# Performance work log

Measured on AMD Instinct MI355X. Metric: run time of the kernel, lower is better.

Reference implementation:

```python
import jax, jax.numpy as jnp
import numpy as np
import math

V, T, E, H, L = 32000, 1024, 1024, 16, 6
B = 2
D = E // H
F = 4 * E


def setup_inputs() -> dict:
    key = jax.random.key(0)
    ks = jax.random.split(key, 12)
    s = 0.02
    rn = lambda k, shape: jax.random.normal(k, shape, jnp.float32) * s
    return dict(
        idx=jax.random.randint(ks[0], (B, T), 0, V),
        tok_w=rn(ks[1], (V, E)),
        pos_w=rn(ks[2], (T, E)),
        ln1_g=jnp.ones((L, E)), ln1_b=jnp.zeros((L, E)),
        wq=rn(ks[3], (L, E, E)), wk=rn(ks[4], (L, E, E)), wv=rn(ks[5], (L, E, E)),
        wp=rn(ks[6], (L, E, E)), bp=jnp.zeros((L, E)),
        ln2_g=jnp.ones((L, E)), ln2_b=jnp.zeros((L, E)),
        w1=rn(ks[7], (L, E, F)), b1=jnp.zeros((L, F)),
        w2=rn(ks[8], (L, F, E)), b2=jnp.zeros((L, E)),
        lnf_g=jnp.ones((E,)), lnf_b=jnp.zeros((E,)),
        wlm=rn(ks[9], (E, V)), blm=jnp.zeros((V,)),
    )


def _layernorm(x, g, b, eps=1e-5):
    m = jnp.mean(x, axis=-1, keepdims=True)
    v = jnp.var(x, axis=-1, keepdims=True)
    return (x - m) * jax.lax.rsqrt(v + eps) * g + b


def _forward(idx, tok_w, pos_w, ln1_g, ln1_b, wq, wk, wv, wp, bp,
             ln2_g, ln2_b, w1, b1, w2, b2, lnf_g, lnf_b, wlm, blm):
    Bx, Tx = idx.shape
    x = tok_w[idx] + pos_w[jnp.arange(Tx)][None, :, :]  # [B,T,E]
    causal = jnp.tril(jnp.ones((Tx, Tx), dtype=bool))
    scale = 1.0 / math.sqrt(D)
    for l in range(L):
        h = _layernorm(x, ln1_g[l], ln1_b[l])
        q = (h @ wq[l]).reshape(Bx, Tx, H, D).transpose(0, 2, 1, 3)  # [B,H,T,D]
        k = (h @ wk[l]).reshape(Bx, Tx, H, D).transpose(0, 2, 1, 3)
        v = (h @ wv[l]).reshape(Bx, Tx, H, D).transpose(0, 2, 1, 3)
        att = jnp.einsum('bhtd,bhsd->bhts', q, k) * scale  # [B,H,T,T]
        att = jnp.where(causal, att, -jnp.inf)
        att = jax.nn.softmax(att, axis=-1)
        y = jnp.einsum('bhts,bhsd->bhtd', att, v)
        y = y.transpose(0, 2, 1, 3).reshape(Bx, Tx, E)
        x = x + y @ wp[l] + bp[l]
        h2 = _layernorm(x, ln2_g[l], ln2_b[l])
        ff = jax.nn.gelu(h2 @ w1[l] + b1[l], approximate=False) @ w2[l] + b2[l]
        x = x + ff
    x = _layernorm(x, lnf_g, lnf_b)
    return x @ wlm + blm  # logits [B,T,V]


def reference(idx, tok_w, pos_w, ln1_g, ln1_b, wq, wk, wv, wp, bp,
              ln2_g, ln2_b, w1, b1, w2, b2, lnf_g, lnf_b, wlm, blm):
    return _forward(idx, tok_w, pos_w, ln1_g, ln1_b, wq, wk, wv, wp, bp,
                    ln2_g, ln2_b, w1, b1, w2, b2, lnf_g, lnf_b, wlm, blm)
```

## Files before the change

### kernel.cpp

```cpp
#include <hip/hip_runtime.h>

#define T_SEQ   1024
#define E_DIM   1024
#define H_HEADS 16
#define D_HEAD  64
#define L_LAYERS 6
#define B_BATCH 2
#define F_DIM   4096
#define V_VOCAB 32000

typedef float f32x4 __attribute__((ext_vector_type(4)));
typedef short short8 __attribute__((ext_vector_type(8)));

__device__ __forceinline__ unsigned short f2bf(float f) {
  union { float f; unsigned int u; } v; v.f = f;
  unsigned int r = v.u + 0x7fffu + ((v.u >> 16) & 1u);
  return (unsigned short)(r >> 16);
}

#define GLDS16(gp, lp) __builtin_amdgcn_global_load_lds( \
    (const __attribute__((address_space(1))) void*)(gp), \
    (__attribute__((address_space(3))) void*)(lp), 16, 0, 0)

__global__ void embed_kernel(const int* __restrict__ idx, const float* __restrict__ tok,
                             const float* __restrict__ pos, float* __restrict__ x) {
  int i = blockIdx.x * 256 + threadIdx.x;
  int bt = i >> 8;
  int e4 = i & 255;
  int t  = bt & (T_SEQ - 1);
  int tokid = idx[bt];
  f32x4 a = *(const f32x4*)(tok + (size_t)tokid * E_DIM + e4 * 4);
  f32x4 p = *(const f32x4*)(pos + (size_t)t * E_DIM + e4 * 4);
  *(f32x4*)(x + (size_t)bt * E_DIM + e4 * 4) = a + p;
}

__global__ void ln_kernel(const float* __restrict__ x, const float* __restrict__ g,
                          const float* __restrict__ b, unsigned short* __restrict__ out) {
  int row = blockIdx.x;
  int tid = threadIdx.x;
  const float* xr = x + (size_t)row * E_DIM;
  f32x4 v = *(const f32x4*)(xr + tid * 4);
  float s  = v[0] + v[1] + v[2] + v[3];
  float s2 = v[0]*v[0] + v[1]*v[1] + v[2]*v[2] + v[3]*v[3];
  #pragma unroll
  for (int off = 32; off > 0; off >>= 1) {
    s  += __shfl_xor(s,  off);
    s2 += __shfl_xor(s2, off);
  }
  __shared__ float red[2][4];
  int wave = tid >> 6;
  if ((tid & 63) == 0) { red[0][wave] = s; red[1][wave] = s2; }
  __syncthreads();
  s  = red[0][0] + red[0][1] + red[0][2] + red[0][3];
  s2 = red[1][0] + red[1][1] + red[1][2] + red[1][3];
  float mean = s * (1.0f / E_DIM);
  float var  = s2 * (1.0f / E_DIM) - mean * mean;
  float rstd = rsqrtf(var + 1e-5f);
  f32x4 gv = *(const f32x4*)(g + tid * 4);
  f32x4 bv = *(const f32x4*)(b + tid * 4);
  ushort4 o;
  o.x = f2bf((v[0] - mean) * rstd * gv[0] + bv[0]);
  o.y = f2bf((v[1] - mean) * rstd * gv[1] + bv[1]);
  o.z = f2bf((v[2] - mean) * rstd * gv[2] + bv[2]);
  o.w = f2bf((v[3] - mean) * rstd * gv[3] + bv[3]);
  *(ushort4*)(out + (size_t)row * E_DIM + tid * 4) = o;
}

__device__ __forceinline__ void wtrans_body(const float* __restrict__ W,
    unsigned short* __restrict__ Wt, int K, int N, int bx, int by) {
  __shared__ float tile[64][65];
  const int n0 = bx * 64, k0 = by * 64;
  const int tr  = threadIdx.x >> 4;
  const int tc4 = (threadIdx.x & 15) * 4;
  #pragma unroll
  for (int p = 0; p < 4; ++p) {
    f32x4 v = *(const f32x4*)(W + (size_t)(k0 + p * 16 + tr) * N + n0 + tc4);
    tile[p * 16 + tr][tc4 + 0] = v[0];
    tile[p * 16 + tr][tc4 + 1] = v[1];
    tile[p * 16 + tr][tc4 + 2] = v[2];
    tile[p * 16 + tr][tc4 + 3] = v[3];
  }
  __syncthreads();
  #pragma unroll
  for (int p = 0; p < 4; ++p) {
    int n = p * 16 + tr;
    ushort4 o;
    o.x = f2bf(tile[tc4 + 0][n]);
    o.y = f2bf(tile[tc4 + 1][n]);
    o.z = f2bf(tile[tc4 + 2][n]);
    o.w = f2bf(tile[tc4 + 3][n]);
    *(ushort4*)(Wt + (size_t)(n0 + n) * K + k0 + tc4) = o;
  }
}

__global__ __launch_bounds__(256) void wtrans_kernel(const float* __restrict__ W,
    unsigned short* __restrict__ Wt, int K, int N) {
  wtrans_body(W, Wt, K, N, blockIdx.x, blockIdx.y);
}

__global__ __launch_bounds__(256) void wtrans6_kernel(const float* __restrict__ wq,
    const float* __restrict__ wk, const float* __restrict__ wv, const float* __restrict__ wp,
    const float* __restrict__ w1, const float* __restrict__ w2,
    unsigned short* __restrict__ wtb) {
  const size_t EE = (size_t)E_DIM * E_DIM;
  const size_t EF = (size_t)E_DIM * F_DIM;
  const int id = blockIdx.x;
  if (id < 1024) {
    const int z = id >> 8, r = id & 255;
    const float* W = z == 0 ? wq : (z == 1 ? wk : (z == 2 ? wv : wp));
    wtrans_body(W, wtb + z * EE, E_DIM, E_DIM, r & 15, r >> 4);
  } else if (id < 2048) {
    const int r = id - 1024;
    wtrans_body(w1, wtb + 4 * EE, E_DIM, F_DIM, r & 63, r >> 6);
  } else {
    const int r = id - 2048;
    wtrans_body(w2, wtb + 4 * EE + EF, F_DIM, E_DIM, r & 15, r >> 4);
  }
}

__global__ __launch_bounds__(512) void attn_mfma_kernel(
    const unsigned short* __restrict__ qk, const unsigned short* __restrict__ vt,
    unsigned short* __restrict__ y) {
  __shared__ __align__(16) char smem[2 * 16384 + 8 * 1280 + 512];
  const int tid  = threadIdx.x;
  const int lane = tid & 63;
  const int wave = tid >> 6;
  const int wl = wave & 3;
  const int g  = wave >> 2;
  const int qx = blockIdx.x;
  const int h  = blockIdx.y & (H_HEADS - 1);
  const int b  = blockIdx.y >> 4;
  const int qt = b ? (15 - qx) : qx;
  const int r0 = qt * 64 + wl * 16;
  const size_t RS = 2 * E_DIM;
  const unsigned short* q  = qk + (size_t)b * T_SEQ * RS + (size_t)h * D_HEAD;
  const unsigned short* k  = q + E_DIM;
  const unsigned short* vb = vt + (size_t)(b * H_HEADS + h) * D_HEAD * T_SEQ;
  const size_t ybase = (size_t)b * T_SEQ * E_DIM + (size_t)h * D_HEAD;
  const int fr = lane & 15, fg = lane >> 4;
  const int srow = lane >> 3;
  const int ssw  = ((lane & 7) * 16) ^ (srow << 4);
  char* pb = smem + 32768 + wave * 1280;
  float* mlb = (float*)(smem + 32768 + 10240);

  short8 aq[2];
  #pragma unroll
  for (int c = 0; c < 2; ++c)
    aq[c] = *(const short8*)(q + (size_t)(r0 + fr) * RS + c * 32 + fg * 8);

  f32x4 oacc[4];
  #pragma unroll
  for (int cg = 0; cg < 4; ++cg) oacc[cg] = (f32x4){0.f, 0.f, 0.f, 0.f};
  float m_ = -1e30f, l_ = 0.0f;

  auto stage = [&](int t) {
    const int j0 = t * 64;
    char* Kd = smem + (t & 1) * 16384;
    GLDS16((const char*)k  + (size_t)(j0 + wave * 8 + srow) * RS * 2 + ssw,
           Kd + wave * 1024);
    GLDS16((const char*)vb + ((size_t)(wave * 8 + srow) * T_SEQ + j0) * 2 + ssw,
           Kd + 8192 + wave * 1024);
  };

  stage(0);
  for (int t = 0; t <= qt; ++t) {
    __builtin_amdgcn_sched_barrier(0);
    __builtin_amdgcn_s_barrier();
    if (t < qt) stage(t + 1);
    __builtin_amdgcn_sched_barrier(0);
    if (t < qt) asm volatile("s_waitcnt vmcnt(2)" ::: "memory");
    else        asm volatile("s_waitcnt vmcnt(0)" ::: "memory");
    __builtin_amdgcn_sched_barrier(0);
    __builtin_amdgcn_s_barrier();
    __builtin_amdgcn_sched_barrier(0);
    const char* Kl = smem + (t & 1) * 16384;
    const char* Vl = Kl + 8192;
    const int j0 = t * 64;
    if (!(t == qt && g == 1 && wl < 2)) {
      f32x4 st[2];
      #pragma unroll
      for (int cc = 0; cc < 2; ++cc) {
        const int kloc = g * 32 + cc * 16 + fr;
        const char* kb = Kl + kloc * 128;
        const int sw = (kloc & 7) << 4;
        short8 ka0 = *(const short8*)(kb + ((fg * 16) ^ sw));
        short8 ka1 = *(const short8*)(kb + ((64 + fg * 16) ^ sw));
        f32x4 z = (f32x4){0.f, 0.f, 0.f, 0.f};
        z = __builtin_amdgcn_mfma_f32_16x16x32_bf16(ka0, aq[0], z, 0, 0, 0);
        z = __builtin_amdgcn_mfma_f32_16x16x32_bf16(ka1, aq[1], z, 0, 0, 0);
        st[cc] = z;
      }
      const int qg = r0 + fr;
      float pv[2][4];
      float mx = -1e30f;
      #pragma unroll
      for (int cc = 0; cc < 2; ++cc)
        #pragma unroll
        for (int r = 0; r < 4; ++r) {
          const int kj = j0 + g * 32 + cc * 16 + fg * 4 + r;
          float val = (kj <= qg) ? st[cc][r] * 0.125f : -1e30f;
          pv[cc][r] = val;
          mx = fmaxf(mx, val);
        }
      mx = fmaxf(mx, __shfl_xor(mx, 16));
      mx = fmaxf(mx, __shfl_xor(mx, 32));
      const float mn = fmaxf(m_, mx);
      const float cfs = __expf(m_ - mn);
      float ls = 0.0f;
      #pragma unroll
      for (int cc = 0; cc < 2; ++cc) {
        ushort4 o;
        float e0 = pv[cc][0] > -1e29f ? __expf(pv[cc][0] - mn) : 0.0f;
        float e1 = pv[cc][1] > -1e29f ? __expf(pv[cc][1] - mn) : 0.0f;
        float e2 = pv[cc][2] > -1e29f ? __expf(pv[cc][2] - mn) : 0.0f;
        float e3 = pv[cc][3] > -1e29f ? __expf(pv[cc][3] - mn) : 0.0f;
        ls += (e0 + e1) + (e2 + e3);
        o.x = f2bf(e0); o.y = f2bf(e1); o.z = f2bf(e2); o.w = f2bf(e3);
        *(ushort4*)(pb + fr * 80 + cc * 32 + fg * 8) = o;
      }
      ls += __shfl_xor(ls, 16);
      ls += __shfl_xor(ls, 32);
      l_ = l_ * cfs + ls;
      m_ = mn;
      float cfO[4];
      #pragma unroll
      for (int r = 0; r < 4; ++r) cfO[r] = __shfl(cfs, (lane & 48) | (fg * 4 + r));
      asm volatile("s_waitcnt lgkmcnt(0)" ::: "memory");
      __builtin_amdgcn_sched_barrier(0);
      short8 pa = *(const short8*)(pb + fr * 80 + fg * 16);
      __builtin_amdgcn_s_setprio(1);
      #pragma unroll
      for (int cg = 0; cg < 4; ++cg) {
        const int d = cg * 16 + fr;
        short8 bv = *(const short8*)(Vl + d * 128 + ((g * 64 + fg * 16) ^ ((d & 7) << 4)));
        #pragma unroll
        for (int r = 0; r < 4; ++r) oacc[cg][r] *= cfO[r];
        oacc[cg] = __builtin_amdgcn_mfma_f32_16x16x32_bf16(pa, bv, oacc[cg], 0, 0, 0);
      }
      __builtin_amdgcn_s_setprio(0);
    }
  }
  __syncthreads();
  float* obuf = (float*)smem;
  if (g == 1) {
    #pragma unroll
    for (int cg = 0; cg < 4; ++cg)
      #pragma unroll
      for (int r = 0; r < 4; ++r)
        obuf[wl * 1024 + (fg * 4 + r) * 64 + cg * 16 + fr] = oacc[cg][r];
    if (fg == 0) { mlb[(wl * 16 + fr) * 2] = m_; mlb[(wl * 16 + fr) * 2 + 1] = l_; }
  }
  __syncthreads();
  if (g == 0) {
    const float m1 = mlb[(wl * 16 + fr) * 2];
    const float l1 = mlb[(wl * 16 + fr) * 2 + 1];
    const float m  = fmaxf(m_, m1);
    const float c0 = __expf(m_ - m), c1 = __expf(m1 - m);
    const float li = 1.0f / (l_ * c0 + l1 * c1);
    float c0O[4], c1O[4], liO[4];
    #pragma unroll
    for (int r = 0; r < 4; ++r) {
      const int src = (lane & 48) | (fg * 4 + r);
      c0O[r] = __shfl(c0, src); c1O[r] = __shfl(c1, src); liO[r] = __shfl(li, src);
    }
    #pragma unroll
    for (int cg = 0; cg < 4; ++cg)
      #pragma unroll
      for (int r = 0; r < 4; ++r) {
        const float o1 = obuf[wl * 1024 + (fg * 4 + r) * 64 + cg * 16 + fr];
        const float val = (oacc[cg][r] * c0O[r] + o1 * c1O[r]) * liO[r];
        y[ybase + (size_t)(r0 + fg * 4 + r) * E_DIM + cg * 16 + fr] = f2bf(val);
      }
  }
}

template<int BM, int BN, bool HAS_BIAS, bool GELU_ACT, bool HAS_RES, int OMODE>
__global__ __launch_bounds__(256) void gemm_bt_kernel(
    const unsigned short* __restrict__ A, const unsigned short* __restrict__ Bt,
    const float* __restrict__ bias, const float* __restrict__ res,
    void* __restrict__ out, unsigned short* __restrict__ vt, int M, int N, int K) {
  constexpr int BK = 64;
  constexpr int MR = BM / 32;
  constexpr int NR = BN / 32;
  constexpr int AI = BM / 32;
  constexpr int BI = BN / 32;
  __shared__ __align__(16) unsigned short As[BM * BK];
  __shared__ __align__(16) unsigned short Bs[BN * BK];
  const int tid  = threadIdx.x;
  const int lane = tid & 63;
  const int wave = tid >> 6;
  const int wr = wave >> 1, wc = wave & 1;

  const int mt = M / BM;
  const int q8 = gridDim.x >> 3;
  const int g  = (blockIdx.x & 7) * q8 + (blockIdx.x >> 3);
  const int m0 = (g % mt) * BM, n0 = (g / mt) * BN;

  const int fr = lane & 15, fg = lane >> 4;
  const int lrow = lane >> 3;
  const int scol = ((lane & 7) * 16) ^ (lrow << 4);
  const size_t K2 = (size_t)K * 2;
  const char* aG = (const char*)A  + (size_t)(m0 + wave * 8 + lrow) * K2 + scol;
  const char* bG = (const char*)Bt + (size_t)(n0 + wave * 8 + lrow) * K2 + scol;

  f32x4 acc[MR][NR];
  #pragma unroll
  for (int mi = 0; mi < MR; ++mi)
    #pragma unroll
    for (int ni = 0; ni < NR; ++ni) acc[mi][ni] = (f32x4){0.f, 0.f, 0.f, 0.f};

  for (int k0 = 0; k0 < K; k0 += BK) {
    __syncthreads();
    #pragma unroll
    for (int i = 0; i < AI; ++i)
      GLDS16(aG + (size_t)i * 32 * K2 + (size_t)k0 * 2, (char*)As + wave * 1024 + i * 4096);
    #pragma unroll
    for (int i = 0; i < BI; ++i)
      GLDS16(bG + (size_t)i * 32 * K2 + (size_t)k0 * 2, (char*)Bs + wave * 1024 + i * 4096);
    __syncthreads();

    short8 af[MR][2], bf[NR][2];
    #pragma unroll
    for (int mi = 0; mi < MR; ++mi) {
      const int row = wr * (BM / 2) + mi * 16 + fr;
      #pragma unroll
      for (int kh = 0; kh < 2; ++kh)
        af[mi][kh] = *(const short8*)((const char*)As + row * 128 +
                       ((kh * 64 + fg * 16) ^ ((row & 7) << 4)));
    }
    #pragma unroll
    for (int ni = 0; ni < NR; ++ni) {
      const int row = wc * (BN / 2) + ni * 16 + fr;
      #pragma unroll
      for (int kh = 0; kh < 2; ++kh)
        bf[ni][kh] = *(const short8*)((const char*)Bs + row * 128 +
                       ((kh * 64 + fg * 16) ^ ((row & 7) << 4)));
    }
    #pragma unroll
    for (int mi = 0; mi < MR; ++mi)
      #pragma unroll
      for (int ni = 0; ni < NR; ++ni) {
        acc[mi][ni] = __builtin_amdgcn_mfma_f32_16x16x32_bf16(af[mi][0], bf[ni][0], acc[mi][ni], 0, 0, 0);
        acc[mi][ni] = __builtin_amdgcn_mfma_f32_16x16x32_bf16(af[mi][1], bf[ni][1], acc[mi][ni], 0, 0, 0);
      }
  }

  #pragma unroll
  for (int mi = 0; mi < MR; ++mi) {
    #pragma unroll
    for (int ni = 0; ni < NR; ++ni) {
      const int col = n0 + wc * (BN / 2) + ni * 16 + fr;
      float bv = HAS_BIAS ? bias[col] : 0.0f;
      float vals[4];
      const int rbase = m0 + wr * (BM / 2) + mi * 16 + fg * 4;
      #pragma unroll
      for (int r = 0; r < 4; ++r) {
        float val = acc[mi][ni][r] + bv;
        if (GELU_ACT) val = 0.5f * val * (1.0f + erff(val * 0.70710678118f));
        if (HAS_RES)  val += res[(size_t)(rbase + r) * N + col];
        vals[r] = val;
      }
      if (OMODE == 0) {
        #pragma unroll
        for (int r = 0; r < 4; ++r)
          ((float*)out)[(size_t)(rbase + r) * N + col] = vals[r];
      } else {
        #pragma unroll
        for (int r = 0; r < 4; ++r)
          ((unsigned short*)out)[(size_t)(rbase + r) * N + col] = f2bf(vals[r]);
      }
    }
  }
}

template<int OMODE, bool HAS_BIAS, bool GELU_ACT>
__global__ __launch_bounds__(512, 1) void gemm8p2_kernel(
    const unsigned short* __restrict__ A, const unsigned short* __restrict__ Bt,
    const float* __restrict__ bias, void* __restrict__ out,
    unsigned short* __restrict__ vt, int M, int N, int K) {
  __shared__ __align__(16) char lds[98304];
  const int tid  = threadIdx.x;
  const int lane = tid & 63;
  const int wv   = tid >> 6;
  const int wm = wv >> 2, wn = wv & 3;

  const int mt = M >> 7;
  const int q8 = gridDim.x >> 3;
  const int g  = (blockIdx.x & 7) * q8 + (blockIdx.x >> 3);
  const int m0 = (g % mt) * 128, n0 = (g / mt) * 256;

  const int fr = lane & 15, fg = lane >> 4;
  const size_t K2 = (size_t)K * 2;
  const int nIter = K >> 7;

  const int csw0 = (fg * 16) ^ ((fr & 7) << 4);
  const int csw1 = (64 + fg * 16) ^ ((fr & 7) << 4);

  const int sc = (lane * 16) & 127;
  const size_t laneoff = (size_t)(lane >> 3) * K2 + (size_t)(sc ^ ((lane >> 3) << 4));
  const char* Asrc = (const char*)(A + (size_t)m0 * K) + laneoff;
  const char* Bsrc = (const char*)(Bt + (size_t)n0 * K) + laneoff;
  const int arow_wv = (wv >> 2) * 64 + (wv & 3) * 8;
  const int brow_wv = (wv >> 2) * 64 + (wv & 3) * 8;

  f32x4 acc[4][4];
  #pragma unroll
  for (int i = 0; i < 4; ++i)
    #pragma unroll
    for (int j = 0; j < 4; ++j) acc[i][j] = (f32x4){0.f, 0.f, 0.f, 0.f};

  auto stageA = [&](int b, int c, int kt) {
    GLDS16(Asrc + (size_t)(arow_wv + c * 32) * K2 + (size_t)kt * 128,
           lds + b * 49152 + c * 8192 + wv * 1024);
  };
  auto stageB = [&](int b, int j, int kt) {
    GLDS16(Bsrc + (size_t)((j & 1) * 128 + (j >> 1) * 32 + brow_wv) * K2 + (size_t)kt * 128,
           lds + b * 49152 + 16384 + j * 8192 + wv * 1024);
  };

  stageA(0, 0, 0); stageA(0, 1, 0);
  stageB(0, 0, 0); stageB(0, 1, 0); stageB(0, 2, 0); stageB(0, 3, 0);
  stageA(1, 0, 1); stageB(1, 0, 1); stageB(1, 1, 1);
  __builtin_amdgcn_sched_barrier(0);
  asm volatile("s_waitcnt vmcnt(3)" ::: "memory");
  __builtin_amdgcn_s_barrier();

  for (int i = 0; i < nIter; ++i) {
    const bool last = (i == nIter - 1);
    #pragma unroll
    for (int p = 0; p < 8; ++p) {
      const int b  = p >> 2;
      const int mh = (p >> 1) & 1;
      const int nh = p & 1;
      const char* Ab = lds + b * 49152;
      const char* Bb = Ab + 16384;
      __builtin_amdgcn_sched_barrier(0);
      short8 fa[2][2], fb[2][2];
      #pragma unroll
      for (int j = 0; j < 2; ++j) {
        const int row = mh * 64 + wm * 32 + j * 16 + fr;
        fa[j][0] = *(const short8*)(Ab + row * 128 + csw0);
        fa[j][1] = *(const short8*)(Ab + row * 128 + csw1);
      }
      #pragma unroll
      for (int n = 0; n < 2; ++n) {
        const int row = nh * 128 + (wn >> 1) * 64 + (wn & 1) * 32 + n * 16 + fr;
        fb[n][0] = *(const short8*)(Bb + row * 128 + csw0);
        fb[n][1] = *(const short8*)(Bb + row * 128 + csw1);
      }
      if (p == 0) stageA(1, 1, 2 * i + 1);
      if (p == 1) { stageB(1, 2, 2 * i + 1); stageB(1, 3, 2 * i + 1); }
      if (!last) {
        if (p == 2) stageA(0, 0, 2 * i + 2);
        if (p == 3) { stageB(0, 0, 2 * i + 2); stageB(0, 1, 2 * i + 2); }
        if (p == 4) stageA(0, 1, 2 * i + 2);
        if (p == 5) { stageB(0, 2, 2 * i + 2); stageB(0, 3, 2 * i + 2); }
        if (p == 6) stageA(1, 0, 2 * i + 3);
        if (p == 7) { stageB(1, 0, 2 * i + 3); stageB(1, 1, 2 * i + 3); }
      }
      __builtin_amdgcn_sched_barrier(0);
      __builtin_amdgcn_s_barrier();
      __builtin_amdgcn_sched_barrier(0);
      __builtin_amdgcn_s_setprio(1);
      #pragma unroll
      for (int j = 0; j < 2; ++j)
        #pragma unroll
        for (int n = 0; n < 2; ++n) {
          acc[mh * 2 + j][nh * 2 + n] = __builtin_amdgcn_mfma_f32_16x16x32_bf16(
              fa[j][0], fb[n][0], acc[mh * 2 + j][nh * 2 + n], 0, 0, 0);
          acc[mh * 2 + j][nh * 2 + n] = __builtin_amdgcn_mfma_f32_16x16x32_bf16(
              fa[j][1], fb[n][1], acc[mh * 2 + j][nh * 2 + n], 0, 0, 0);
        }
      __builtin_amdgcn_s_setprio(0);
      __builtin_amdgcn_sched_barrier(0);
      if (p == 3) {
        if (!last) asm volatile("s_waitcnt vmcnt(3)" ::: "memory");
        else       asm volatile("s_waitcnt vmcnt(0)" ::: "memory");
      }
      if (p == 7 && !last)
        asm volatile("s_waitcnt vmcnt(3)" ::: "memory");
      __builtin_amdgcn_s_barrier();
    }
  }

  #pragma unroll
  for (int mi = 0; mi < 4; ++mi) {
    #pragma unroll
    for (int ni = 0; ni < 4; ++ni) {
      const int col = n0 + wn * 64 + ni * 16 + fr;
      float bv = HAS_BIAS ? bias[col] : 0.0f;
      const int rbase = m0 + wm * 64 + mi * 16 + fg * 4;
      float vals[4];
      #pragma unroll
      for (int r = 0; r < 4; ++r) {
        float val = acc[mi][ni][r] + bv;
        if (GELU_ACT) val = 0.5f * val * (1.0f + erff(val * 0.70710678118f));
        vals[r] = val;
      }
      if (OMODE == 1) {
        #pragma unroll
        for (int r = 0; r < 4; ++r)
          ((unsigned short*)out)[(size_t)(rbase + r) * N + col] = f2bf(vals[r]);
      } else {
        if (col < 2 * E_DIM) {
          #pragma unroll
          for (int r = 0; r < 4; ++r)
            ((unsigned short*)out)[(size_t)(rbase + r) * 2 * E_DIM + col] = f2bf(vals[r]);
        } else {
          const int c2 = col - 2 * E_DIM;
          const int hh = c2 >> 6, d = c2 & 63;
          const int bb = rbase >> 10, t0 = rbase & (T_SEQ - 1);
          ushort4 o;
          o.x = f2bf(vals[0]); o.y = f2bf(vals[1]);
          o.z = f2bf(vals[2]); o.w = f2bf(vals[3]);
          *(ushort4*)(vt + ((size_t)(bb * H_HEADS + hh) * D_HEAD + d) * T_SEQ + t0) = o;
        }
      }
    }
  }
}

__global__ __launch_bounds__(512, 1) void gemm8p_kernel(
    const unsigned short* __restrict__ A, const unsigned short* __restrict__ Bt,
    const float* __restrict__ bias, float* __restrict__ out, int M, int N, int K) {
  __shared__ __align__(16) char lds[131072];
  const int tid  = threadIdx.x;
  const int lane = tid & 63;
  const int wv   = tid >> 6;
  const int wm = wv >> 2, wn = wv & 3;

  const int mt = M >> 8;
  const int q8 = gridDim.x >> 3;
  const int g  = (blockIdx.x & 7) * q8 + (blockIdx.x >> 3);
  const int m0 = (g % mt) * 256, n0 = (g / mt) * 256;

  const int fr = lane & 15, fg = lane >> 4;
  const size_t K2 = (size_t)K * 2;
  const int nIter = K >> 7;

  const int csw0 = (fg * 16) ^ ((fr & 7) << 4);
  const int csw1 = (64 + fg * 16) ^ ((fr & 7) << 4);

  const int sc = (lane * 16) & 127;
  const size_t laneoff = (size_t)(lane >> 3) * K2 + (size_t)(sc ^ ((lane >> 3) << 4));
  const char* Asrc = (const char*)(A + (size_t)m0 * K) + (size_t)(wv * 8) * K2 + laneoff;
  const char* Bsrc = (const char*)(Bt + (size_t)n0 * K) + laneoff;

  f32x4 acc[8][4];
  #pragma unroll
  for (int i = 0; i < 8; ++i)
    #pragma unroll
    for (int j = 0; j < 4; ++j) acc[i][j] = (f32x4){0.f, 0.f, 0.f, 0.f};

  auto stageA = [&](int b, int q, int kt) {
    GLDS16(Asrc + (size_t)(q * 64) * K2 + (size_t)kt * 128,
           lds + b * 65536 + q * 8192 + wv * 1024);
  };
  auto stageB = [&](int b, int j, int o, int kt) {
    const int gw = j * 64 + wv * 8;
    const int rw = ((gw >> 5) << 6) + (gw & 31) + o * 32;
    GLDS16(Bsrc + (size_t)rw * K2 + (size_t)kt * 128,
           lds + b * 65536 + 32768 + rw * 128);
  };

  stageA(0, 0, 0); stageA(0, 2, 0);
  stageB(0, 0, 0, 0); stageB(0, 1, 0, 0);
  stageA(0, 1, 0); stageA(0, 3, 0);
  stageB(0, 0, 1, 0); stageB(0, 1, 1, 0);
  stageA(1, 0, 1); stageA(1, 2, 1);
  stageB(1, 0, 0, 1); stageB(1, 1, 0, 1);
  __builtin_amdgcn_sched_barrier(0);
  asm volatile("s_waitcnt vmcnt(4)" ::: "memory");
  __builtin_amdgcn_s_barrier();

  for (int i = 0; i < nIter; ++i) {
    const bool last = (i == nIter - 1);
    #pragma unroll
    for (int p = 0; p < 8; ++p) {
      const int b  = p >> 2;
      const int mh = (p & 3) >> 1;
      const int nh = p & 1;
      const char* Ab = lds + b * 65536;
      const char* Bb = Ab + 32768;
      __builtin_amdgcn_sched_barrier(0);
      short8 fa[4][2], fb[2][2];
      #pragma unroll
      for (int j = 0; j < 4; ++j) {
        const int row = wm * 128 + mh * 64 + j * 16 + fr;
        fa[j][0] = *(const short8*)(Ab + row * 128 + csw0);
        fa[j][1] = *(const short8*)(Ab + row * 128 + csw1);
      }
      #pragma unroll
      for (int n = 0; n < 2; ++n) {
        const int row = wn * 64 + nh * 32 + n * 16 + fr;
        fb[n][0] = *(const short8*)(Bb + row * 128 + csw0);
        fb[n][1] = *(const short8*)(Bb + row * 128 + csw1);
      }
      if (p == 0) { stageA(1, 1, 2 * i + 1); stageA(1, 3, 2 * i + 1); }
      if (p == 1) { stageB(1, 0, 1, 2 * i + 1); stageB(1, 1, 1, 2 * i + 1); }
      if (!last) {
        if (p == 2) { stageA(0, 0, 2 * i + 2); stageA(0, 2, 2 * i + 2); }
        if (p == 3) { stageB(0, 0, 0, 2 * i + 2); stageB(0, 1, 0, 2 * i + 2); }
        if (p == 4) { stageA(0, 1, 2 * i + 2); stageA(0, 3, 2 * i + 2); }
        if (p == 5) { stageB(0, 0, 1, 2 * i + 2); stageB(0, 1, 1, 2 * i + 2); }
        if (p == 6) { stageA(1, 0, 2 * i + 3); stageA(1, 2, 2 * i + 3); }
        if (p == 7) { stageB(1, 0, 0, 2 * i + 3); stageB(1, 1, 0, 2 * i + 3); }
      }
      __builtin_amdgcn_sched_barrier(0);
      __builtin_amdgcn_s_barrier();
      __builtin_amdgcn_sched_barrier(0);
      __builtin_amdgcn_s_setprio(1);
      #pragma unroll
      for (int j = 0; j < 4; ++j)
        #pragma unroll
        for (int n = 0; n < 2; ++n) {
          acc[mh * 4 + j][nh * 2 + n] = __builtin_amdgcn_mfma_f32_16x16x32_bf16(
              fa[j][0], fb[n][0], acc[mh * 4 + j][nh * 2 + n], 0, 0, 0);
          acc[mh * 4 + j][nh * 2 + n] = __builtin_amdgcn_mfma_f32_16x16x32_bf16(
              fa[j][1], fb[n][1], acc[mh * 4 + j][nh * 2 + n], 0, 0, 0);
        }
      __builtin_amdgcn_s_setprio(0);
      __builtin_amdgcn_sched_barrier(0);
      if (p == 3) {
        if (!last) asm volatile("s_waitcnt vmcnt(4)" ::: "memory");
        else       asm volatile("s_waitcnt vmcnt(0)" ::: "memory");
      }
      if (p == 7 && !last)
        asm volatile("s_waitcnt vmcnt(4)" ::: "memory");
      __builtin_amdgcn_s_barrier();
    }
  }

  #pragma unroll
  for (int mi = 0; mi < 8; ++mi) {
    #pragma unroll
    for (int ni = 0; ni < 4; ++ni) {
      const int col = n0 + wn * 64 + ni * 16 + fr;
      const float bv = bias[col];
      #pragma unroll
      for (int r = 0; r < 4; ++r) {
        const int row = m0 + wm * 128 + mi * 16 + fg * 4 + r;
        out[(size_t)row * N + col] = acc[mi][ni][r] + bv;
      }
    }
  }
}

extern "C" void kernel_launch(void* const* d_in, const int* in_sizes, int n_in,
                              void* d_out, int out_size, void* d_ws, size_t ws_size,
                              hipStream_t stream) {
  const int*   idx   = (const int*)  d_in[0];
  const float* tok_w = (const float*)d_in[1];
  const float* pos_w = (const float*)d_in[2];
  const float* ln1_g = (const float*)d_in[3];
  const float* ln1_b = (const float*)d_in[4];
  const float* wq    = (const float*)d_in[5];
  const float* wk    = (const float*)d_in[6];
  const float* wv    = (const float*)d_in[7];
  const float* wp    = (const float*)d_in[8];
  const float* bp    = (const float*)d_in[9];
  const float* ln2_g = (const float*)d_in[10];
  const float* ln2_b = (const float*)d_in[11];
  const float* w1    = (const float*)d_in[12];
  const float* b1    = (const float*)d_in[13];
  const float* w2    = (const float*)d_in[14];
  const float* b2    = (const float*)d_in[15];
  const float* lnf_g = (const float*)d_in[16];
  const float* lnf_b = (const float*)d_in[17];
  const float* wlm   = (const float*)d_in[18];
  const float* blm   = (const float*)d_in[19];

  const int M = B_BATCH * T_SEQ;
  const size_t EE = (size_t)E_DIM * E_DIM;
  const size_t EF = (size_t)E_DIM * F_DIM;
  char* p = (char*)d_ws;
  float* x            = (float*)p;          p += (size_t)M * E_DIM * 4;
  unsigned short* hb  = (unsigned short*)p; p += (size_t)M * E_DIM * 2;
  unsigned short* qkb = (unsigned short*)p; p += (size_t)M * 2 * E_DIM * 2;
  unsigned short* vtb = (unsigned short*)p; p += (size_t)M * E_DIM * 2;
  unsigned short* yb  = (unsigned short*)p; p += (size_t)M * E_DIM * 2;
  unsigned short* tb  = (unsigned short*)p; p += (size_t)M * F_DIM * 2;
  unsigned short* wtb = (unsigned short*)p; p += (size_t)V_VOCAB * E_DIM * 2;

  embed_kernel<<<M * E_DIM / 4 / 256, 256, 0, stream>>>(idx, tok_w, pos_w, x);

  for (int l = 0; l < L_LAYERS; ++l) {
    wtrans6_kernel<<<3072, 256, 0, stream>>>(
        wq + l * EE, wk + l * EE, wv + l * EE, wp + l * EE,
        w1 + l * EF, w2 + l * EF, wtb);
    ln_kernel<<<M, 256, 0, stream>>>(x, ln1_g + (size_t)l * E_DIM, ln1_b + (size_t)l * E_DIM, hb);
    gemm8p2_kernel<2, false, false>
        <<<(M / 128) * (3 * E_DIM / 256), 512, 0, stream>>>(
        hb, wtb, nullptr, qkb, vtb, M, 3 * E_DIM, E_DIM);
    attn_mfma_kernel<<<dim3(16, B_BATCH * H_HEADS), 512, 0, stream>>>(qkb, vtb, yb);
    gemm_bt_kernel<64, 128, true, false, true, 0>
        <<<(M / 64) * (E_DIM / 128), 256, 0, stream>>>(
        yb, wtb + 3 * EE, bp + (size_t)l * E_DIM, x, x, nullptr, M, E_DIM, E_DIM);
    ln_kernel<<<M, 256, 0, stream>>>(x, ln2_g + (size_t)l * E_DIM, ln2_b + (size_t)l * E_DIM, hb);
    gemm8p2_kernel<1, true, true>
        <<<(M / 128) * (F_DIM / 256), 512, 0, stream>>>(
        hb, wtb + 4 * EE, b1 + (size_t)l * F_DIM, tb, nullptr, M, F_DIM, E_DIM);
    gemm_bt_kernel<64, 128, true, false, true, 0>
        <<<(M / 64) * (E_DIM / 128), 256, 0, stream>>>(
        tb, wtb + 4 * EE + EF, b2 + (size_t)l * E_DIM, x, x, nullptr, M, E_DIM, F_DIM);
  }
  ln_kernel<<<M, 256, 0, stream>>>(x, lnf_g, lnf_b, hb);
  wtrans_kernel<<<dim3(V_VOCAB / 64, E_DIM / 64), 256, 0, stream>>>(wlm, wtb, E_DIM, V_VOCAB);
  gemm8p_kernel<<<(M / 256) * (V_VOCAB / 256), 512, 0, stream>>>(
      hb, wtb, blm, (float*)d_out, M, V_VOCAB, E_DIM);
}
```

Before: 1.297 ms.

## Stage GEMM epilogues through LDS for vector stores; merge layernorm into weight-transpose launches

Rewrites the epilogues of the three GEMM kernels so each wave first writes its accumulator tile into a padded LDS scratch area. It then reads the tile back row-wise and emits 16-byte (fp32) or 8-byte (bf16) vectorised global stores, with vectorised residual loads, instead of scattered scalar stores. Separately, the layernorm launches are folded into the weight-transpose kernels as extra blocks, both per layer and for the final LM head, removing kernel launches. This adds LDS reuse after the main loop, with explicit waitcnt and sched barriers, and makes the grids heterogeneous.

New measurement: 1.292 ms. Within noise of the previous version (-0.4%).

```diff
diff --git a/kernel.cpp b/kernel.cpp
--- a/kernel.cpp
+++ b/kernel.cpp
@@ -34,9 +34,9 @@
   *(f32x4*)(x + (size_t)bt * E_DIM + e4 * 4) = a + p;
 }
 
-__global__ void ln_kernel(const float* __restrict__ x, const float* __restrict__ g,
-                          const float* __restrict__ b, unsigned short* __restrict__ out) {
-  int row = blockIdx.x;
+__device__ __forceinline__ void ln_body(const float* __restrict__ x,
+    const float* __restrict__ g, const float* __restrict__ b,
+    unsigned short* __restrict__ out, int row) {
   int tid = threadIdx.x;
   const float* xr = x + (size_t)row * E_DIM;
   f32x4 v = *(const f32x4*)(xr + tid * 4);
@@ -66,6 +66,11 @@
   *(ushort4*)(out + (size_t)row * E_DIM + tid * 4) = o;
 }
 
+__global__ void ln_kernel(const float* __restrict__ x, const float* __restrict__ g,
+                          const float* __restrict__ b, unsigned short* __restrict__ out) {
+  ln_body(x, g, b, out, blockIdx.x);
+}
+
 __device__ __forceinline__ void wtrans_body(const float* __restrict__ W,
     unsigned short* __restrict__ Wt, int K, int N, int bx, int by) {
   __shared__ float tile[64][65];
@@ -93,15 +98,12 @@
   }
 }
 
-__global__ __launch_bounds__(256) void wtrans_kernel(const float* __restrict__ W,
-    unsigned short* __restrict__ Wt, int K, int N) {
-  wtrans_body(W, Wt, K, N, blockIdx.x, blockIdx.y);
-}
-
-__global__ __launch_bounds__(256) void wtrans6_kernel(const float* __restrict__ wq,
+__global__ __launch_bounds__(256) void wtrans6ln_kernel(const float* __restrict__ wq,
     const float* __restrict__ wk, const float* __restrict__ wv, const float* __restrict__ wp,
     const float* __restrict__ w1, const float* __restrict__ w2,
-    unsigned short* __restrict__ wtb) {
+    const float* __restrict__ lng, const float* __restrict__ lnb,
+    const float* __restrict__ x, unsigned short* __restrict__ wtb,
+    unsigned short* __restrict__ hb) {
   const size_t EE = (size_t)E_DIM * E_DIM;
   const size_t EF = (size_t)E_DIM * F_DIM;
   const int id = blockIdx.x;
@@ -112,10 +114,21 @@
   } else if (id < 2048) {
     const int r = id - 1024;
     wtrans_body(w1, wtb + 4 * EE, E_DIM, F_DIM, r & 63, r >> 6);
-  } else {
+  } else if (id < 3072) {
     const int r = id - 2048;
     wtrans_body(w2, wtb + 4 * EE + EF, F_DIM, E_DIM, r & 15, r >> 4);
-  }
+  } else {
+    ln_body(x, lng, lnb, hb, id - 3072);
+  }
+}
+
+__global__ __launch_bounds__(256) void wtransv_ln_kernel(const float* __restrict__ wlm,
+    const float* __restrict__ lng, const float* __restrict__ lnb,
+    const float* __restrict__ x, unsigned short* __restrict__ wtb,
+    unsigned short* __restrict__ hb) {
+  const int id = blockIdx.x;
+  if (id < 8000) wtrans_body(wlm, wtb, E_DIM, V_VOCAB, id % 500, id / 500);
+  else           ln_body(x, lng, lnb, hb, id - 8000);
 }
 
 __global__ __launch_bounds__(512) void attn_mfma_kernel(
@@ -284,8 +297,9 @@
   constexpr int NR = BN / 32;
   constexpr int AI = BM / 32;
   constexpr int BI = BN / 32;
-  __shared__ __align__(16) unsigned short As[BM * BK];
-  __shared__ __align__(16) unsigned short Bs[BN * BK];
+  __shared__ __align__(16) char smem[(BM + BN) * BK * 2];
+  unsigned short* As = (unsigned short*)smem;
+  unsigned short* Bs = (unsigned short*)(smem + (size_t)BM * BK * 2);
   const int tid  = threadIdx.x;
   const int lane = tid & 63;
   const int wave = tid >> 6;
@@ -345,31 +359,52 @@
       }
   }
 
-  #pragma unroll
-  for (int mi = 0; mi < MR; ++mi) {
-    #pragma unroll
-    for (int ni = 0; ni < NR; ++ni) {
-      const int col = n0 + wc * (BN / 2) + ni * 16 + fr;
-      float bv = HAS_BIAS ? bias[col] : 0.0f;
-      float vals[4];
-      const int rbase = m0 + wr * (BM / 2) + mi * 16 + fg * 4;
-      #pragma unroll
-      for (int r = 0; r < 4; ++r) {
-        float val = acc[mi][ni][r] + bv;
-        if (GELU_ACT) val = 0.5f * val * (1.0f + erff(val * 0.70710678118f));
-        if (HAS_RES)  val += res[(size_t)(rbase + r) * N + col];
-        vals[r] = val;
-      }
-      if (OMODE == 0) {
+  if (OMODE == 0) {
+    __syncthreads();
+    float* tw = (float*)(smem + wave * 4352);
+    float bv4[NR];
+    #pragma unroll
+    for (int ni = 0; ni < NR; ++ni)
+      bv4[ni] = HAS_BIAS ? bias[n0 + wc * (BN / 2) + ni * 16 + fr] : 0.0f;
+    #pragma unroll
+    for (int mi = 0; mi < MR; ++mi) {
+      #pragma unroll
+      for (int ni = 0; ni < NR; ++ni)
         #pragma unroll
-        for (int r = 0; r < 4; ++r)
-          ((float*)out)[(size_t)(rbase + r) * N + col] = vals[r];
-      } else {
+        for (int r = 0; r < 4; ++r) {
+          float val = acc[mi][ni][r] + bv4[ni];
+          if (GELU_ACT) val = 0.5f * val * (1.0f + erff(val * 0.70710678118f));
+          tw[(fg * 4 + r) * 68 + ni * 16 + fr] = val;
+        }
+      asm volatile("s_waitcnt lgkmcnt(0)" ::: "memory");
+      __builtin_amdgcn_sched_barrier(0);
+      #pragma unroll
+      for (int rr = 0; rr < 4; ++rr) {
+        const int row = rr * 4 + (lane >> 4);
+        const int grow = m0 + wr * (BM / 2) + mi * 16 + row;
+        const int gcol = n0 + wc * (BN / 2) + (lane & 15) * 4;
+        f32x4 v = *(const f32x4*)&tw[row * 68 + (lane & 15) * 4];
+        if (HAS_RES) v += *(const f32x4*)(res + (size_t)grow * N + gcol);
+        *(f32x4*)((float*)out + (size_t)grow * N + gcol) = v;
+      }
+      asm volatile("s_waitcnt lgkmcnt(0)" ::: "memory");
+      __builtin_amdgcn_sched_barrier(0);
+    }
+  } else {
+    #pragma unroll
+    for (int mi = 0; mi < MR; ++mi)
+      #pragma unroll
+      for (int ni = 0; ni < NR; ++ni) {
+        const int col = n0 + wc * (BN / 2) + ni * 16 + fr;
+        float bv = HAS_BIAS ? bias[col] : 0.0f;
+        const int rbase = m0 + wr * (BM / 2) + mi * 16 + fg * 4;
         #pragma unroll
-        for (int r = 0; r < 4; ++r)
-          ((unsigned short*)out)[(size_t)(rbase + r) * N + col] = f2bf(vals[r]);
-      }
-    }
+        for (int r = 0; r < 4; ++r) {
+          float val = acc[mi][ni][r] + bv;
+          if (GELU_ACT) val = 0.5f * val * (1.0f + erff(val * 0.70710678118f));
+          ((unsigned short*)out)[(size_t)(rbase + r) * N + col] = f2bf(val);
+        }
+      }
   }
 }
 
@@ -483,25 +518,46 @@
     }
   }
 
-  #pragma unroll
-  for (int mi = 0; mi < 4; ++mi) {
-    #pragma unroll
-    for (int ni = 0; ni < 4; ++ni) {
-      const int col = n0 + wn * 64 + ni * 16 + fr;
-      float bv = HAS_BIAS ? bias[col] : 0.0f;
-      const int rbase = m0 + wm * 64 + mi * 16 + fg * 4;
-      float vals[4];
-      #pragma unroll
-      for (int r = 0; r < 4; ++r) {
-        float val = acc[mi][ni][r] + bv;
-        if (GELU_ACT) val = 0.5f * val * (1.0f + erff(val * 0.70710678118f));
-        vals[r] = val;
-      }
-      if (OMODE == 1) {
+  if (OMODE == 1) {
+    unsigned short* tw = (unsigned short*)(lds + wv * 2176);
+    float bv4[4];
+    #pragma unroll
+    for (int ni = 0; ni < 4; ++ni)
+      bv4[ni] = HAS_BIAS ? bias[n0 + wn * 64 + ni * 16 + fr] : 0.0f;
+    #pragma unroll
+    for (int mi = 0; mi < 4; ++mi) {
+      #pragma unroll
+      for (int ni = 0; ni < 4; ++ni)
         #pragma unroll
-        for (int r = 0; r < 4; ++r)
-          ((unsigned short*)out)[(size_t)(rbase + r) * N + col] = f2bf(vals[r]);
-      } else {
+        for (int r = 0; r < 4; ++r) {
+          float val = acc[mi][ni][r] + bv4[ni];
+          if (GELU_ACT) val = 0.5f * val * (1.0f + erff(val * 0.70710678118f));
+          tw[(fg * 4 + r) * 68 + ni * 16 + fr] = f2bf(val);
+        }
+      asm volatile("s_waitcnt lgkmcnt(0)" ::: "memory");
+      __builtin_amdgcn_sched_barrier(0);
+      #pragma unroll
+      for (int rr = 0; rr < 4; ++rr) {
+        const int row = rr * 4 + (lane >> 4);
+        const int grow = m0 + wm * 64 + mi * 16 + row;
+        const int gcol = n0 + wn * 64 + (lane & 15) * 4;
+        ushort4 v = *(const ushort4*)&tw[row * 68 + (lane & 15) * 4];
+        *(ushort4*)((unsigned short*)out + (size_t)grow * N + gcol) = v;
+      }
+      asm volatile("s_waitcnt lgkmcnt(0)" ::: "memory");
+      __builtin_amdgcn_sched_barrier(0);
+    }
+  } else {
+    #pragma unroll
+    for (int mi = 0; mi < 4; ++mi) {
+      #pragma unroll
+      for (int ni = 0; ni < 4; ++ni) {
+        const int col = n0 + wn * 64 + ni * 16 + fr;
+        float bv = HAS_BIAS ? bias[col] : 0.0f;
+        const int rbase = m0 + wm * 64 + mi * 16 + fg * 4;
+        float vals[4];
+        #pragma unroll
+        for (int r = 0; r < 4; ++r) vals[r] = acc[mi][ni][r] + bv;
         if (col < 2 * E_DIM) {
           #pragma unroll
           for (int r = 0; r < 4; ++r)
@@ -631,18 +687,29 @@
     }
   }
 
+  float* tw = (float*)(lds + wv * 4352);
+  float bv4[4];
+  #pragma unroll
+  for (int ni = 0; ni < 4; ++ni) bv4[ni] = bias[n0 + wn * 64 + ni * 16 + fr];
   #pragma unroll
   for (int mi = 0; mi < 8; ++mi) {
     #pragma unroll
-    for (int ni = 0; ni < 4; ++ni) {
-      const int col = n0 + wn * 64 + ni * 16 + fr;
-      const float bv = bias[col];
-      #pragma unroll
-      for (int r = 0; r < 4; ++r) {
-        const int row = m0 + wm * 128 + mi * 16 + fg * 4 + r;
-        out[(size_t)row * N + col] = acc[mi][ni][r] + bv;
-      }
-    }
+    for (int ni = 0; ni < 4; ++ni)
+      #pragma unroll
+      for (int r = 0; r < 4; ++r)
+        tw[(fg * 4 + r) * 68 + ni * 16 + fr] = acc[mi][ni][r] + bv4[ni];
+    asm volatile("s_waitcnt lgkmcnt(0)" ::: "memory");
+    __builtin_amdgcn_sched_barrier(0);
+    #pragma unroll
+    for (int rr = 0; rr < 4; ++rr) {
+      const int row = rr * 4 + (lane >> 4);
+      const int grow = m0 + wm * 128 + mi * 16 + row;
+      const int gcol = n0 + wn * 64 + (lane & 15) * 4;
+      f32x4 v = *(const f32x4*)&tw[row * 68 + (lane & 15) * 4];
+      *(f32x4*)(out + (size_t)grow * N + gcol) = v;
+    }
+    asm volatile("s_waitcnt lgkmcnt(0)" ::: "memory");
+    __builtin_amdgcn_sched_barrier(0);
   }
 }
 
@@ -685,10 +752,10 @@
   embed_kernel<<<M * E_DIM / 4 / 256, 256, 0, stream>>>(idx, tok_w, pos_w, x);
 
   for (int l = 0; l < L_LAYERS; ++l) {
-    wtrans6_kernel<<<3072, 256, 0, stream>>>(
+    wtrans6ln_kernel<<<5120, 256, 0, stream>>>(
         wq + l * EE, wk + l * EE, wv + l * EE, wp + l * EE,
-        w1 + l * EF, w2 + l * EF, wtb);
-    ln_kernel<<<M, 256, 0, stream>>>(x, ln1_g + (size_t)l * E_DIM, ln1_b + (size_t)l * E_DIM, hb);
+        w1 + l * EF, w2 + l * EF,
+        ln1_g + (size_t)l * E_DIM, ln1_b + (size_t)l * E_DIM, x, wtb, hb);
     gemm8p2_kernel<2, false, false>
         <<<(M / 128) * (3 * E_DIM / 256), 512, 0, stream>>>(
         hb, wtb, nullptr, qkb, vtb, M, 3 * E_DIM, E_DIM);
@@ -704,8 +771,7 @@
         <<<(M / 64) * (E_DIM / 128), 256, 0, stream>>>(
         tb, wtb + 4 * EE + EF, b2 + (size_t)l * E_DIM, x, x, nullptr, M, E_DIM, F_DIM);
   }
-  ln_kernel<<<M, 256, 0, stream>>>(x, lnf_g, lnf_b, hb);
-  wtrans_kernel<<<dim3(V_VOCAB / 64, E_DIM / 64), 256, 0, stream>>>(wlm, wtb, E_DIM, V_VOCAB);
+  wtransv_ln_kernel<<<10048, 256, 0, stream>>>(wlm, lnf_g, lnf_b, x, wtb, hb);
   gemm8p_kernel<<<(M / 256) * (V_VOCAB / 256), 512, 0, stream>>>(
       hb, wtb, blm, (float*)d_out, M, V_VOCAB, E_DIM);
 }
```
